# Performance work log

Measured on AMD Instinct MI355X. Metric: run time of the kernel, lower is better.

The kernel has to match this reference:

```python
import jax, jax.numpy as jnp
import numpy as np

EPS = 1e-5

def _layer_norm(x, g, b):
    mu = jnp.mean(x, axis=-1, keepdims=True)
    var = jnp.mean((x - mu) ** 2, axis=-1, keepdims=True)
    return (x - mu) * jax.lax.rsqrt(var + EPS) * g + b

def _aggregate(x, ei, emask):
    # x: [N, D], ei: [2, E], emask: [E] (0/1 float). Mean over valid incoming edges.
    N = x.shape[0]
    src, tgt = ei[0], ei[1]
    valid = emask > 0
    tgt_eff = jnp.where(valid, tgt, N)  # route masked edges to dummy segment
    msgs = x[src] * emask[:, None]      # [E, D]
    sums = jax.ops.segment_sum(msgs, tgt_eff, num_segments=N + 1)[:N]
    cnt = jax.ops.segment_sum(emask, tgt_eff, num_segments=N + 1)[:N]
    return sums / jnp.maximum(cnt, 1.0)[:, None]

def _forward(node_feats, edge_index, node_mask, edge_mask,
             in_W, in_b, self_W, self_b, neigh_W, neigh_b, ln_g, ln_b,
             out1_W, out1_b, out2_W, out2_b):
    x = jax.nn.relu(node_feats @ in_W + in_b)  # [B, N, H]
    L = self_W.shape[0]
    agg_fn = jax.vmap(_aggregate)
    for l in range(L):
        self_feats = x @ self_W[l] + self_b[l]
        neigh = agg_fn(x, edge_index, edge_mask)
        neigh_feats = neigh @ neigh_W[l] + neigh_b[l]
        h = jax.nn.relu(self_feats + neigh_feats)
        h = _layer_norm(h, ln_g[l], ln_b[l])
        x = h * node_mask[:, :, None]
    # global mean_max pool
    masked = x * node_mask[:, :, None]
    n_valid = jnp.maximum(jnp.sum(node_mask, axis=1, keepdims=True), 1.0)
    mean_pool = jnp.sum(masked, axis=1) / n_valid
    neg_inf = jnp.asarray(-jnp.inf, x.dtype)
    max_pool = jnp.max(jnp.where(node_mask[:, :, None] > 0, masked, neg_inf), axis=1)
    g = jnp.concatenate([mean_pool, max_pool], axis=1)  # [B, 2H]
    h = jax.nn.relu(g @ out1_W + out1_b)
    return h @ out2_W + out2_b  # [B, output_dim]

def setup_inputs() -> dict:
    key = jax.random.key(0)
    ks = jax.random.split(key, 12)
    B, N, E = 8, 8192, 65536
    F_IN, H, OUT, L = 64, 128, 256, 3
    inp = {}
    inp['graph_node_feats'] = jax.random.normal(ks[0], (B, N, F_IN), jnp.float32)
    inp['graph_edge_index'] = jax.random.randint(ks[1], (B, 2, E), 0, N, jnp.int32)
    inp['graph_node_mask'] = jnp.ones((B, N), jnp.float32)
    inp['graph_edge_mask'] = jnp.ones((B, E), jnp.float32)
    s = lambda k, sh, fan: jax.random.normal(k, sh, jnp.float32) * (1.0 / np.sqrt(fan))
    inp['in_W'] = s(ks[2], (F_IN, H), F_IN)
    inp['in_b'] = jnp.zeros((H,), jnp.float32)
    inp['self_W'] = s(ks[3], (L, H, H), H)
    inp['self_b'] = jnp.zeros((L, H), jnp.float32)
    inp['neigh_W'] = s(ks[4], (L, H, H), H)
    inp['neigh_b'] = jnp.zeros((L, H), jnp.float32)
    inp['ln_g'] = jnp.ones((L, H), jnp.float32)
    inp['ln_b'] = jnp.zeros((L, H), jnp.float32)
    inp['out1_W'] = s(ks[5], (2 * H, H), 2 * H)
    inp['out1_b'] = jnp.zeros((H,), jnp.float32)
    inp['out2_W'] = s(ks[6], (H, OUT), H)
    inp['out2_b'] = jnp.zeros((OUT,), jnp.float32)
    return inp

def reference(graph_node_feats, graph_edge_index, graph_node_mask, graph_edge_mask,
              in_W, in_b, self_W, self_b, neigh_W, neigh_b, ln_g, ln_b,
              out1_W, out1_b, out2_W, out2_b):
    return _forward(graph_node_feats, graph_edge_index, graph_node_mask, graph_edge_mask,
                    in_W, in_b, self_W, self_b, neigh_W, neigh_b, ln_g, ln_b,
                    out1_W, out1_b, out2_W, out2_b)
```

## Files before the change

kernel.cpp:

```cpp
#include <hip/hip_runtime.h>
#include <hip/hip_bf16.h>

#define B 8
#define N 8192
#define E 65536
#define FIN 64
#define H 128
#define OUTD 256
#define NLAYER 3
#define EPS 1e-5f
#define PCHUNK 64
#define PNODES (N / PCHUNK)
#define NNODE (B * N)
#define KSTEPS 8
#define BPL (KSTEPS * 8 * 512)
#define INSTEPS 6
#define ELLW 48

#define AS1 __attribute__((address_space(1)))
#define AS3 __attribute__((address_space(3)))

typedef float f32x4 __attribute__((ext_vector_type(4)));
typedef __bf16 bf16x8 __attribute__((ext_vector_type(8)));

__device__ __forceinline__ float b2f(unsigned short u) {
    union { float f; unsigned int i; } c; c.i = ((unsigned int)u) << 16; return c.f;
}
__device__ __forceinline__ unsigned short f2b(float f) {
    __hip_bfloat16 h = __float2bfloat16(f);
    return *reinterpret_cast<unsigned short*>(&h);
}

__global__ void k_prep(const float* __restrict__ selfW, const float* __restrict__ neighW,
                       const float* __restrict__ inW,
                       unsigned short* __restrict__ Bp, unsigned short* __restrict__ Bpi) {
    const int idx = blockIdx.x;
    const int lane = threadIdx.x;
    const int quad = lane >> 4, col = lane & 15;
    if (idx < NLAYER * KSTEPS * 8) {
        const int t = idx & 7;
        const int s = (idx >> 3) % KSTEPS;
        const int l = idx / (KSTEPS * 8);
        const int g = s >> 2;
        const float* W = ((g == 0) ? selfW : neighW) + (size_t)l * H * H;
        const int n = t * 16 + col;
        unsigned short* dst = Bp + ((size_t)(l * KSTEPS + s) * 8 + t) * 512 + lane * 8;
        #pragma unroll
        for (int j = 0; j < 8; ++j) {
            const int kk = (s & 3) * 32 + quad * 8 + j;
            dst[j] = f2b(W[kk * H + n]);
        }
    } else {
        const int idx2 = idx - NLAYER * KSTEPS * 8;
        const int t = idx2 & 7;
        const int s = idx2 >> 3;
        const int g = s >> 1;
        const bool lo = (g == 2);
        const int n = t * 16 + col;
        unsigned short* dst = Bpi + ((size_t)(s * 8 + t)) * 512 + lane * 8;
        #pragma unroll
        for (int j = 0; j < 8; ++j) {
            const int kk = (s & 1) * 32 + quad * 8 + j;
            const float w = inW[kk * H + n];
            const unsigned short hi = f2b(w);
            dst[j] = lo ? f2b(w - b2f(hi)) : hi;
        }
    }
}

__global__ __launch_bounds__(256) void k_inproj5(const float* __restrict__ feats,
                                                 const unsigned short* __restrict__ Bpi,
                                                 const float* __restrict__ bias,
                                                 unsigned short* __restrict__ xh) {
    const int tid = threadIdx.x;
    const int wv = tid >> 6, lane = tid & 63;
    const int quad = lane >> 4, col = lane & 15;
    const int mg = wv >> 1, nw = wv & 1;
    const int row0 = blockIdx.x * 64;

    bf16x8 fh[2][2], fl[2][2];
    #pragma unroll
    for (int mt = 0; mt < 2; ++mt) {
        const int row = row0 + (mg * 2 + mt) * 16 + col;
        #pragma unroll
        for (int j = 0; j < 2; ++j) {
            const float* src = &feats[(size_t)row * FIN + j * 32 + quad * 8];
            const float4 v0 = *(const float4*)src;
            const float4 v1 = *(const float4*)(src + 4);
            const float fv[8] = {v0.x, v0.y, v0.z, v0.w, v1.x, v1.y, v1.z, v1.w};
            union { bf16x8 v; unsigned short u[8]; } Hh, Ll;
            #pragma unroll
            for (int q = 0; q < 8; ++q) {
                const unsigned short hu = f2b(fv[q]);
                Hh.u[q] = hu;
                Ll.u[q] = f2b(fv[q] - b2f(hu));
            }
            fh[mt][j] = Hh.v;
            fl[mt][j] = Ll.v;
        }
    }

    f32x4 acc[2][4] = {};
    bf16x8 bC[4];
    #pragma unroll
    for (int nt = 0; nt < 4; ++nt)
        bC[nt] = *(const bf16x8*)&Bpi[((size_t)(nw * 4 + nt)) * 512 + lane * 8];

    #pragma unroll
    for (int s = 0; s < INSTEPS; ++s) {
        bf16x8 bN[4];
        if (s + 1 < INSTEPS) {
            #pragma unroll
            for (int nt = 0; nt < 4; ++nt)
                bN[nt] = *(const bf16x8*)&Bpi[((size_t)(s + 1) * 8 + nw * 4 + nt) * 512 + lane * 8];
        }
        const int g = s >> 1, j = s & 1;
        #pragma unroll
        for (int mt = 0; mt < 2; ++mt) {
            const bf16x8 a = (g == 1) ? fl[mt][j] : fh[mt][j];
            #pragma unroll
            for (int nt = 0; nt < 4; ++nt)
                acc[mt][nt] = __builtin_amdgcn_mfma_f32_16x16x32_bf16(a, bC[nt], acc[mt][nt], 0, 0, 0);
        }
        #pragma unroll
        for (int nt = 0; nt < 4; ++nt) bC[nt] = bN[nt];
    }

    #pragma unroll
    for (int nt = 0; nt < 4; ++nt) {
        const int hh = (nw * 4 + nt) * 16 + col;
        const float bv = bias[hh];
        #pragma unroll
        for (int mt = 0; mt < 2; ++mt)
            #pragma unroll
            for (int r = 0; r < 4; ++r) {
                const int row = row0 + (mg * 2 + mt) * 16 + quad * 4 + r;
                const float y = fmaxf(acc[mt][nt][r] + bv, 0.f);
                xh[(size_t)row * H + hh] = f2b(y);
            }
    }
}

__global__ void k_fill_ell(const int* __restrict__ ei, const float* __restrict__ emask,
                           int* __restrict__ ecnt, unsigned int* __restrict__ ell) {
    const int ge = blockIdx.x * 256 + threadIdx.x;
    const float m = emask[ge];
    if (m > 0.f) {
        const int b = ge >> 16, e = ge & 0xFFFF;
        const int tgt = ei[(b * 2 + 1) * E + e];
        const int src = ei[(b * 2) * E + e];
        const int r = b * N + tgt;
        const int p = atomicAdd(&ecnt[r], 1);
        if (p < ELLW)
            ell[(size_t)r * ELLW + p] = ((unsigned int)f2b(m) << 16) | (unsigned int)src;
    }
}

__global__ __launch_bounds__(256) void k_gather6(const unsigned int* __restrict__ xh32,
                                                 const int* __restrict__ ecnt,
                                                 const unsigned int* __restrict__ ell,
                                                 unsigned int* __restrict__ nh32) {
    const int beta = blockIdx.x;
    const int b = beta & 7;
    const int grp = beta >> 3;
    const int wave = threadIdx.x >> 6, lane = threadIdx.x & 63;
    const int r = b * N + grp * 4 + wave;
    const int cnt = min(ecnt[r], ELLW);
    unsigned int pv = 0;
    if (lane < cnt) pv = ell[(size_t)r * ELLW + lane];
    const size_t bbase = (size_t)b * N * 64;
    float a0 = 0.f, a1 = 0.f, c = 0.f;
    const int cnt4 = (cnt + 3) & ~3;
    for (int jj = 0; jj < cnt4; jj += 4) {
        #pragma unroll
        for (int q = 0; q < 4; ++q) {
            const unsigned int pk = __shfl(pv, jj + q);
            const float m = b2f((unsigned short)(pk >> 16));
            const unsigned int u = xh32[bbase + (size_t)(pk & 0xFFFFu) * 64 + lane];
            union { unsigned int i; float f; } lo, hi;
            lo.i = u << 16;
            hi.i = u & 0xFFFF0000u;
            a0 = fmaf(lo.f, m, a0);
            a1 = fmaf(hi.f, m, a1);
            c += m;
        }
    }
    const float inv = 1.f / fmaxf(c, 1.f);
    nh32[(size_t)r * 64 + lane] = (unsigned int)f2b(a0 * inv) | ((unsigned int)f2b(a1 * inv) << 16);
}

__global__ __launch_bounds__(256) void k_layer8(const unsigned short* __restrict__ xinh,
                                                const unsigned short* __restrict__ nh,
                                                const unsigned short* __restrict__ Bp,
                                                const float* __restrict__ sb,
                                                const float* __restrict__ nb,
                                                const float* __restrict__ lng,
                                                const float* __restrict__ lnb,
                                                const float* __restrict__ nmask,
                                                unsigned short* __restrict__ oxh) {
    __shared__ __align__(16) unsigned short bbuf[2][16 * 512];
    __shared__ float lsum[2][64];
    __shared__ float lsq[2][64];

    const int tid = threadIdx.x;
    const int wv = tid >> 6, lane = tid & 63;
    const int quad = lane >> 4, col = lane & 15;
    const int mg = wv >> 1, nw = wv & 1;
    const int u = blockIdx.x;
    const int b = u & 7;
    const int row0 = b * N + (u >> 3) * 64;

    size_t abase[2];
    #pragma unroll
    for (int mt = 0; mt < 2; ++mt)
        abase[mt] = (size_t)(row0 + (mg * 2 + mt) * 16 + col) * H + quad * 8;

    #pragma unroll
    for (int i = 0; i < 4; ++i) {
        const unsigned short* g = Bp + (size_t)(wv * 4 + i) * 512 + lane * 8;
        __builtin_amdgcn_global_load_lds((const AS1 unsigned int*)g,
                                         (AS3 unsigned int*)&bbuf[0][(wv * 4 + i) * 512],
                                         16, 0, 0);
    }
    bf16x8 aC[2][2];
    #pragma unroll
    for (int j = 0; j < 2; ++j)
        #pragma unroll
        for (int mt = 0; mt < 2; ++mt)
            aC[j][mt] = *(const bf16x8*)&xinh[abase[mt] + j * 32];

    f32x4 acc[2][4] = {};

    #pragma unroll
    for (int c = 0; c < 4; ++c) {
        __syncthreads();
        bf16x8 aN[2][2];
        if (c < 3) {
            const int c1 = c + 1;
            #pragma unroll
            for (int i = 0; i < 4; ++i) {
                const unsigned short* g = Bp + (size_t)(c1 * 16 + wv * 4 + i) * 512 + lane * 8;
                __builtin_amdgcn_global_load_lds((const AS1 unsigned int*)g,
                                                 (AS3 unsigned int*)&bbuf[c1 & 1][(wv * 4 + i) * 512],
                                                 16, 0, 0);
            }
            const unsigned short* A1 = (c1 < 2) ? xinh : nh;
            #pragma unroll
            for (int j = 0; j < 2; ++j)
                #pragma unroll
                for (int mt = 0; mt < 2; ++mt)
                    aN[j][mt] = *(const bf16x8*)&A1[abase[mt] + ((c1 & 1) * 2 + j) * 32];
        }
        #pragma unroll
        for (int j = 0; j < 2; ++j) {
            bf16x8 bf[4];
            #pragma unroll
            for (int nt = 0; nt < 4; ++nt)
                bf[nt] = *(const bf16x8*)&bbuf[c & 1][(j * 8 + nw * 4 + nt) * 512 + lane * 8];
            #pragma unroll
            for (int mt = 0; mt < 2; ++mt)
                #pragma unroll
                for (int nt = 0; nt < 4; ++nt)
                    acc[mt][nt] = __builtin_amdgcn_mfma_f32_16x16x32_bf16(aC[j][mt], bf[nt], acc[mt][nt], 0, 0, 0);
        }
        #pragma unroll
        for (int j = 0; j < 2; ++j)
            #pragma unroll
            for (int mt = 0; mt < 2; ++mt)
                aC[j][mt] = aN[j][mt];
    }

    float sbv[4], nbv[4], gv[4], bbv[4];
    #pragma unroll
    for (int nt = 0; nt < 4; ++nt) {
        const int hh = (nw * 4 + nt) * 16 + col;
        sbv[nt] = sb[hh]; nbv[nt] = nb[hh]; gv[nt] = lng[hh]; bbv[nt] = lnb[hh];
    }
    #pragma unroll
    for (int mt = 0; mt < 2; ++mt)
        #pragma unroll
        for (int nt = 0; nt < 4; ++nt)
            #pragma unroll
            for (int r = 0; r < 4; ++r)
                acc[mt][nt][r] = fmaxf(acc[mt][nt][r] + sbv[nt] + nbv[nt], 0.f);

    #pragma unroll
    for (int mt = 0; mt < 2; ++mt)
        #pragma unroll
        for (int r = 0; r < 4; ++r) {
            float p = 0.f, q = 0.f;
            #pragma unroll
            for (int nt = 0; nt < 4; ++nt) {
                const float v = acc[mt][nt][r];
                p += v;
                q = fmaf(v, v, q);
            }
            p += __shfl_xor(p, 1);  q += __shfl_xor(q, 1);
            p += __shfl_xor(p, 2);  q += __shfl_xor(q, 2);
            p += __shfl_xor(p, 4);  q += __shfl_xor(q, 4);
            p += __shfl_xor(p, 8);  q += __shfl_xor(q, 8);
            if (col == 0) {
                const int rib = (mg * 2 + mt) * 16 + quad * 4 + r;
                lsum[nw][rib] = p;
                lsq[nw][rib] = q;
            }
        }
    __syncthreads();

    #pragma unroll
    for (int mt = 0; mt < 2; ++mt)
        #pragma unroll
        for (int r = 0; r < 4; ++r) {
            const int rib = (mg * 2 + mt) * 16 + quad * 4 + r;
            const int node = row0 + rib;
            const float mu = (lsum[0][rib] + lsum[1][rib]) * (1.f / H);
            const float var = (lsq[0][rib] + lsq[1][rib]) * (1.f / H) - mu * mu;
            const float isd = rsqrtf(var + EPS);
            const float m = nmask[node];
            #pragma unroll
            for (int nt = 0; nt < 4; ++nt) {
                const float y = (fmaf(acc[mt][nt][r] - mu, isd * gv[nt], bbv[nt])) * m;
                oxh[(size_t)node * H + (nw * 4 + nt) * 16 + col] = f2b(y);
            }
        }
}

__global__ void k_pool1(const unsigned short* __restrict__ xh,
                        const float* __restrict__ nmask, float* __restrict__ part) {
    const int b = blockIdx.x, c = blockIdx.y, h = threadIdx.x;
    const int n0 = c * PNODES;
    float s = 0.f, mx = -INFINITY, nv = 0.f;
    for (int it = 0; it < PNODES; ++it) {
        const int n = n0 + it;
        const float m = nmask[b * N + n];
        const float v = b2f(xh[((size_t)b * N + n) * H + h]) * m;
        s += v;
        if (m > 0.f) mx = fmaxf(mx, v);
        nv += m;
    }
    float* p = part + ((size_t)b * PCHUNK + c) * (2 * H + 1);
    p[h] = s;
    p[H + h] = mx;
    if (h == 0) p[2 * H] = nv;
}

__global__ __launch_bounds__(256) void k_tail(const float* __restrict__ part,
                                              const float* __restrict__ W1, const float* __restrict__ b1,
                                              const float* __restrict__ W2, const float* __restrict__ b2,
                                              float* __restrict__ out) {
    const int b = blockIdx.x, t = threadIdx.x;
    __shared__ float g[2 * H];
    __shared__ float hid[H];
    {
        float nv = 0.f;
        for (int c = 0; c < PCHUNK; ++c)
            nv += part[((size_t)b * PCHUNK + c) * (2 * H + 1) + 2 * H];
        if (t < H) {
            float s = 0.f;
            for (int c = 0; c < PCHUNK; ++c)
                s += part[((size_t)b * PCHUNK + c) * (2 * H + 1) + t];
            g[t] = s / fmaxf(nv, 1.f);
        } else {
            const int h = t - H;
            float mx = -INFINITY;
            for (int c = 0; c < PCHUNK; ++c)
                mx = fmaxf(mx, part[((size_t)b * PCHUNK + c) * (2 * H + 1) + H + h]);
            g[t] = mx;
        }
    }
    __syncthreads();
    if (t < H) {
        float a = b1[t];
        #pragma unroll 8
        for (int k = 0; k < 2 * H; ++k) a = fmaf(g[k], W1[k * H + t], a);
        hid[t] = fmaxf(a, 0.f);
    }
    __syncthreads();
    float a = b2[t];
    #pragma unroll 8
    for (int k = 0; k < H; ++k) a = fmaf(hid[k], W2[k * OUTD + t], a);
    out[(size_t)b * OUTD + t] = a;
}

extern "C" void kernel_launch(void* const* d_in, const int* in_sizes, int n_in,
                              void* d_out, int out_size, void* d_ws, size_t ws_size,
                              hipStream_t stream) {
    const float* feats = (const float*)d_in[0];
    const int*   ei    = (const int*)d_in[1];
    const float* nmask = (const float*)d_in[2];
    const float* emask = (const float*)d_in[3];
    const float* inW   = (const float*)d_in[4];
    const float* inb   = (const float*)d_in[5];
    const float* selfW = (const float*)d_in[6];
    const float* selfb = (const float*)d_in[7];
    const float* neighW= (const float*)d_in[8];
    const float* neighb= (const float*)d_in[9];
    const float* lng   = (const float*)d_in[10];
    const float* lnb   = (const float*)d_in[11];
    const float* W1    = (const float*)d_in[12];
    const float* b1    = (const float*)d_in[13];
    const float* W2    = (const float*)d_in[14];
    const float* b2    = (const float*)d_in[15];
    float* out = (float*)d_out;

    const size_t nxh = (size_t)NNODE * H;
    char* w = (char*)d_ws;
    unsigned short* xh  = (unsigned short*)w;  w += nxh * 2;
    unsigned short* nh  = (unsigned short*)w;  w += nxh * 2;
    unsigned short* Bp  = (unsigned short*)w;  w += (size_t)NLAYER * BPL * 2;
    unsigned short* Bpi = (unsigned short*)w;  w += (size_t)INSTEPS * 8 * 512 * 2;
    float* part = (float*)w;                   w += (size_t)B * PCHUNK * (2 * H + 1) * 4;
    int* ecnt   = (int*)w;                     w += (size_t)NNODE * 4;
    unsigned int* ell = (unsigned int*)w;      w += (size_t)NNODE * ELLW * 4;

    k_prep<<<NLAYER * KSTEPS * 8 + INSTEPS * 8, 64, 0, stream>>>(selfW, neighW, inW, Bp, Bpi);
    k_inproj5<<<NNODE / 64, 256, 0, stream>>>(feats, Bpi, inb, xh);

    hipMemsetAsync(ecnt, 0, (size_t)NNODE * sizeof(int), stream);
    k_fill_ell<<<B * E / 256, 256, 0, stream>>>(ei, emask, ecnt, ell);

    for (int l = 0; l < NLAYER; ++l) {
        k_gather6<<<NNODE / 4, 256, 0, stream>>>((const unsigned int*)xh, ecnt, ell,
                                                 (unsigned int*)nh);
        k_layer8<<<NNODE / 64, 256, 0, stream>>>(xh, nh,
                                                 Bp + (size_t)l * BPL,
                                                 selfb + (size_t)l * H, neighb + (size_t)l * H,
                                                 lng + (size_t)l * H, lnb + (size_t)l * H,
                                                 nmask, xh);
    }

    k_pool1<<<dim3(B, PCHUNK), H, 0, stream>>>(xh, nmask, part);
    k_tail<<<B, 256, 0, stream>>>(part, W1, b1, W2, b2, out);
}
```

Measured before the change: 283.3 us.

## Fuse ELL fill into input projection and pooling into last layer kernel

The edge-to-ELL fill is merged into the input-projection kernel as extra blocks, so one launch covers both. Mean/max pooling now happens in the epilogue of the last layer kernel, which skips writing the final activations and drops the separate pool kernel. The gather kernel loads the ELL row unconditionally before reading the count and unrolls by 8 instead of 4. This trades launch overhead and one full activation read/write for extra epilogue logic and more partial-sum chunks for the tail kernel to reduce.

After: 280.4 us. Within noise of the previous version (-1.0%).

```diff
diff --git a/kernel.cpp b/kernel.cpp
--- a/kernel.cpp
+++ b/kernel.cpp
@@ -9,8 +9,7 @@
 #define OUTD 256
 #define NLAYER 3
 #define EPS 1e-5f
-#define PCHUNK 64
-#define PNODES (N / PCHUNK)
+#define NCHUNK 128
 #define NNODE (B * N)
 #define KSTEPS 8
 #define BPL (KSTEPS * 8 * 512)
@@ -68,11 +67,29 @@
     }
 }
 
-__global__ __launch_bounds__(256) void k_inproj5(const float* __restrict__ feats,
-                                                 const unsigned short* __restrict__ Bpi,
-                                                 const float* __restrict__ bias,
-                                                 unsigned short* __restrict__ xh) {
+__global__ __launch_bounds__(256) void k_front(const float* __restrict__ feats,
+                                               const unsigned short* __restrict__ Bpi,
+                                               const float* __restrict__ bias,
+                                               unsigned short* __restrict__ xh,
+                                               const int* __restrict__ ei,
+                                               const float* __restrict__ emask,
+                                               int* __restrict__ ecnt,
+                                               unsigned int* __restrict__ ell) {
     const int tid = threadIdx.x;
+    if (blockIdx.x >= 1024) {
+        const int ge = (blockIdx.x - 1024) * 256 + tid;
+        const float m = emask[ge];
+        if (m > 0.f) {
+            const int b = ge >> 16, e = ge & 0xFFFF;
+            const int tgt = ei[(b * 2 + 1) * E + e];
+            const int src = ei[(b * 2) * E + e];
+            const int r = b * N + tgt;
+            const int p = atomicAdd(&ecnt[r], 1);
+            if (p < ELLW)
+                ell[(size_t)r * ELLW + p] = ((unsigned int)f2b(m) << 16) | (unsigned int)src;
+        }
+        return;
+    }
     const int wv = tid >> 6, lane = tid & 63;
     const int quad = lane >> 4, col = lane & 15;
     const int mg = wv >> 1, nw = wv & 1;
@@ -141,22 +158,7 @@
     }
 }
 
-__global__ void k_fill_ell(const int* __restrict__ ei, const float* __restrict__ emask,
-                           int* __restrict__ ecnt, unsigned int* __restrict__ ell) {
-    const int ge = blockIdx.x * 256 + threadIdx.x;
-    const float m = emask[ge];
-    if (m > 0.f) {
-        const int b = ge >> 16, e = ge & 0xFFFF;
-        const int tgt = ei[(b * 2 + 1) * E + e];
-        const int src = ei[(b * 2) * E + e];
-        const int r = b * N + tgt;
-        const int p = atomicAdd(&ecnt[r], 1);
-        if (p < ELLW)
-            ell[(size_t)r * ELLW + p] = ((unsigned int)f2b(m) << 16) | (unsigned int)src;
-    }
-}
-
-__global__ __launch_bounds__(256) void k_gather6(const unsigned int* __restrict__ xh32,
+__global__ __launch_bounds__(256) void k_gather7(const unsigned int* __restrict__ xh32,
                                                  const int* __restrict__ ecnt,
                                                  const unsigned int* __restrict__ ell,
                                                  unsigned int* __restrict__ nh32) {
@@ -165,15 +167,16 @@
     const int grp = beta >> 3;
     const int wave = threadIdx.x >> 6, lane = threadIdx.x & 63;
     const int r = b * N + grp * 4 + wave;
+    unsigned int pv = 0;
+    if (lane < ELLW) pv = ell[(size_t)r * ELLW + lane];
     const int cnt = min(ecnt[r], ELLW);
-    unsigned int pv = 0;
-    if (lane < cnt) pv = ell[(size_t)r * ELLW + lane];
+    if (lane >= cnt) pv = 0;
     const size_t bbase = (size_t)b * N * 64;
     float a0 = 0.f, a1 = 0.f, c = 0.f;
-    const int cnt4 = (cnt + 3) & ~3;
-    for (int jj = 0; jj < cnt4; jj += 4) {
-        #pragma unroll
-        for (int q = 0; q < 4; ++q) {
+    const int cnt8 = (cnt + 7) & ~7;
+    for (int jj = 0; jj < cnt8; jj += 8) {
+        #pragma unroll
+        for (int q = 0; q < 8; ++q) {
             const unsigned int pk = __shfl(pv, jj + q);
             const float m = b2f((unsigned short)(pk >> 16));
             const unsigned int u = xh32[bbase + (size_t)(pk & 0xFFFFu) * 64 + lane];
@@ -189,7 +192,7 @@
     nh32[(size_t)r * 64 + lane] = (unsigned int)f2b(a0 * inv) | ((unsigned int)f2b(a1 * inv) << 16);
 }
 
-__global__ __launch_bounds__(256) void k_layer8(const unsigned short* __restrict__ xinh,
+__global__ __launch_bounds__(256) void k_layer9(const unsigned short* __restrict__ xinh,
                                                 const unsigned short* __restrict__ nh,
                                                 const unsigned short* __restrict__ Bp,
                                                 const float* __restrict__ sb,
@@ -197,10 +200,14 @@
                                                 const float* __restrict__ lng,
                                                 const float* __restrict__ lnb,
                                                 const float* __restrict__ nmask,
-                                                unsigned short* __restrict__ oxh) {
+                                                unsigned short* __restrict__ oxh,
+                                                float* __restrict__ part,
+                                                const int last) {
     __shared__ __align__(16) unsigned short bbuf[2][16 * 512];
     __shared__ float lsum[2][64];
     __shared__ float lsq[2][64];
+    __shared__ float psum_s[2][H];
+    __shared__ float pmax_s[2][H];
 
     const int tid = threadIdx.x;
     const int wv = tid >> 6, lane = tid & 63;
@@ -208,7 +215,8 @@
     const int mg = wv >> 1, nw = wv & 1;
     const int u = blockIdx.x;
     const int b = u & 7;
-    const int row0 = b * N + (u >> 3) * 64;
+    const int chunk = u >> 3;
+    const int row0 = b * N + chunk * 64;
 
     size_t abase[2];
     #pragma unroll
@@ -307,6 +315,9 @@
         }
     __syncthreads();
 
+    float psum[4] = {0.f, 0.f, 0.f, 0.f};
+    float pmax[4] = {-INFINITY, -INFINITY, -INFINITY, -INFINITY};
+
     #pragma unroll
     for (int mt = 0; mt < 2; ++mt)
         #pragma unroll
@@ -320,28 +331,44 @@
             #pragma unroll
             for (int nt = 0; nt < 4; ++nt) {
                 const float y = (fmaf(acc[mt][nt][r] - mu, isd * gv[nt], bbv[nt])) * m;
-                oxh[(size_t)node * H + (nw * 4 + nt) * 16 + col] = f2b(y);
-            }
-        }
-}
-
-__global__ void k_pool1(const unsigned short* __restrict__ xh,
-                        const float* __restrict__ nmask, float* __restrict__ part) {
-    const int b = blockIdx.x, c = blockIdx.y, h = threadIdx.x;
-    const int n0 = c * PNODES;
-    float s = 0.f, mx = -INFINITY, nv = 0.f;
-    for (int it = 0; it < PNODES; ++it) {
-        const int n = n0 + it;
-        const float m = nmask[b * N + n];
-        const float v = b2f(xh[((size_t)b * N + n) * H + h]) * m;
-        s += v;
-        if (m > 0.f) mx = fmaxf(mx, v);
-        nv += m;
-    }
-    float* p = part + ((size_t)b * PCHUNK + c) * (2 * H + 1);
-    p[h] = s;
-    p[H + h] = mx;
-    if (h == 0) p[2 * H] = nv;
+                if (!last) {
+                    oxh[(size_t)node * H + (nw * 4 + nt) * 16 + col] = f2b(y);
+                } else {
+                    psum[nt] += y;
+                    pmax[nt] = fmaxf(pmax[nt], (m > 0.f) ? y : -INFINITY);
+                }
+            }
+        }
+
+    if (last) {
+        #pragma unroll
+        for (int nt = 0; nt < 4; ++nt) {
+            psum[nt] += __shfl_xor(psum[nt], 16);
+            psum[nt] += __shfl_xor(psum[nt], 32);
+            pmax[nt] = fmaxf(pmax[nt], __shfl_xor(pmax[nt], 16));
+            pmax[nt] = fmaxf(pmax[nt], __shfl_xor(pmax[nt], 32));
+        }
+        if (quad == 0)
+            #pragma unroll
+            for (int nt = 0; nt < 4; ++nt) {
+                psum_s[mg][(nw * 4 + nt) * 16 + col] = psum[nt];
+                pmax_s[mg][(nw * 4 + nt) * 16 + col] = pmax[nt];
+            }
+        float nv = 0.f;
+        if (wv == 0) {
+            nv = nmask[row0 + lane];
+            nv += __shfl_xor(nv, 1);  nv += __shfl_xor(nv, 2);
+            nv += __shfl_xor(nv, 4);  nv += __shfl_xor(nv, 8);
+            nv += __shfl_xor(nv, 16); nv += __shfl_xor(nv, 32);
+        }
+        __syncthreads();
+        float* p = part + ((size_t)b * NCHUNK + chunk) * (2 * H + 1);
+        if (tid < H) {
+            p[tid] = psum_s[0][tid] + psum_s[1][tid];
+            p[H + tid] = fmaxf(pmax_s[0][tid], pmax_s[1][tid]);
+        }
+        if (tid == 0) p[2 * H] = nv;
+    }
 }
 
 __global__ __launch_bounds__(256) void k_tail(const float* __restrict__ part,
@@ -353,18 +380,18 @@
     __shared__ float hid[H];
     {
         float nv = 0.f;
-        for (int c = 0; c < PCHUNK; ++c)
-            nv += part[((size_t)b * PCHUNK + c) * (2 * H + 1) + 2 * H];
+        for (int c = 0; c < NCHUNK; ++c)
+            nv += part[((size_t)b * NCHUNK + c) * (2 * H + 1) + 2 * H];
         if (t < H) {
             float s = 0.f;
-            for (int c = 0; c < PCHUNK; ++c)
-                s += part[((size_t)b * PCHUNK + c) * (2 * H + 1) + t];
+            for (int c = 0; c < NCHUNK; ++c)
+                s += part[((size_t)b * NCHUNK + c) * (2 * H + 1) + t];
             g[t] = s / fmaxf(nv, 1.f);
         } else {
             const int h = t - H;
             float mx = -INFINITY;
-            for (int c = 0; c < PCHUNK; ++c)
-                mx = fmaxf(mx, part[((size_t)b * PCHUNK + c) * (2 * H + 1) + H + h]);
+            for (int c = 0; c < NCHUNK; ++c)
+                mx = fmaxf(mx, part[((size_t)b * NCHUNK + c) * (2 * H + 1) + H + h]);
             g[t] = mx;
         }
     }
@@ -409,26 +436,23 @@
     unsigned short* nh  = (unsigned short*)w;  w += nxh * 2;
     unsigned short* Bp  = (unsigned short*)w;  w += (size_t)NLAYER * BPL * 2;
     unsigned short* Bpi = (unsigned short*)w;  w += (size_t)INSTEPS * 8 * 512 * 2;
-    float* part = (float*)w;                   w += (size_t)B * PCHUNK * (2 * H + 1) * 4;
+    float* part = (float*)w;                   w += (size_t)B * NCHUNK * (2 * H + 1) * 4;
     int* ecnt   = (int*)w;                     w += (size_t)NNODE * 4;
     unsigned int* ell = (unsigned int*)w;      w += (size_t)NNODE * ELLW * 4;
 
     k_prep<<<NLAYER * KSTEPS * 8 + INSTEPS * 8, 64, 0, stream>>>(selfW, neighW, inW, Bp, Bpi);
-    k_inproj5<<<NNODE / 64, 256, 0, stream>>>(feats, Bpi, inb, xh);
-
     hipMemsetAsync(ecnt, 0, (size_t)NNODE * sizeof(int), stream);
-    k_fill_ell<<<B * E / 256, 256, 0, stream>>>(ei, emask, ecnt, ell);
+    k_front<<<1024 + B * E / 256, 256, 0, stream>>>(feats, Bpi, inb, xh, ei, emask, ecnt, ell);
 
     for (int l = 0; l < NLAYER; ++l) {
-        k_gather6<<<NNODE / 4, 256, 0, stream>>>((const unsigned int*)xh, ecnt, ell,
+        k_gather7<<<NNODE / 4, 256, 0, stream>>>((const unsigned int*)xh, ecnt, ell,
                                                  (unsigned int*)nh);
-        k_layer8<<<NNODE / 64, 256, 0, stream>>>(xh, nh,
+        k_layer9<<<NNODE / 64, 256, 0, stream>>>(xh, nh,
                                                  Bp + (size_t)l * BPL,
                                                  selfb + (size_t)l * H, neighb + (size_t)l * H,
                                                  lng + (size_t)l * H, lnb + (size_t)l * H,
-                                                 nmask, xh);
-    }
-
-    k_pool1<<<dim3(B, PCHUNK), H, 0, stream>>>(xh, nmask, part);
+                                                 nmask, xh, part, (l == NLAYER - 1) ? 1 : 0);
+    }
+
     k_tail<<<B, 256, 0, stream>>>(part, W1, b1, W2, b2, out);
 }
```
